# Kernel tuning notes

Hardware: AMD Instinct MI355X
Metric: run time of the kernel (lower is better)

The kernel has to match this reference:

```python
import jax, jax.numpy as jnp
import numpy as np

T, K, D, CIN = 8, 64, 512, 1536  # timesteps, num_centers, redu_dim, input channels


def _conv(x, w, b=None, pad=0):
    y = jax.lax.conv_general_dilated(x, w, (1, 1), [(pad, pad), (pad, pad)],
                                     dimension_numbers=('NCHW', 'OIHW', 'NCHW'))
    return y if b is None else y + b[None, :, None, None]


def setup_inputs() -> dict:
    key = jax.random.key(0)
    ks = jax.random.split(key, 15)
    B, H, W = 32, 8, 8
    s = lambda i, shp: jax.random.normal(ks[i], shp, jnp.float32) * 0.05
    return dict(
        x=jax.random.normal(ks[0], (B * T, CIN, H, W), jnp.float32),
        redu_w=s(1, (D, CIN, 1, 1)), redu_b=s(2, (D,)),
        w_x=s(3, (K, D, 1, 1)),
        att_x=s(4, (K, K, 3, 3)), att_h_w=s(5, (K, K, 3, 3)), att_b=s(6, (K,)),
        share_w=s(7, (K, K, 3, 3)), share_b=s(8, (K,)),
        U_r=s(9, (K, K, 3, 3)), U_z=s(10, (K, K, 3, 3)), U_h=s(11, (K, K, 3, 3)),
        centers=s(12, (K, D)),
        fc1_w=s(13, (T * K // 16, T * K)), fc2_w=s(14, (T * K, T * K // 16)),
    )


def reference(x, redu_w, redu_b, w_x, att_x, att_h_w, att_b, share_w, share_b,
              U_r, U_z, U_h, centers, fc1_w, fc2_w):
    NT, _, H, W = x.shape
    B = NT // T
    xt = _conv(x, redu_w, redu_b)                    # (B*T, D, H, W) 1x1 reduction
    wxpb = _conv(xt, w_x)                            # (B*T, K, H, W)
    att_v = _conv(wxpb, att_x, pad=1).reshape(B, T, K, H, W).transpose(1, 0, 2, 3, 4)  # (T,B,K,H,W)
    wxpb5 = wxpb.reshape(B, T, K, H, W)

    def fc(v):  # ChannelAttention shared MLP (1x1 convs == matmuls)
        return jnp.maximum(v @ fc1_w.T, 0.) @ fc2_w.T

    def step(h, _):
        ah = _conv(h, att_h_w, att_b, pad=1)               # (B,K,H,W)
        e = jax.nn.relu(att_v + ah[None])                  # (T,B,K,H,W)
        e = e.transpose(1, 0, 2, 3, 4).reshape(B, T * K, H * W)
        g = jnp.tanh(fc(e.mean(-1)) + fc(e.max(-1)))       # (B, T*K) channel attention
        ex = jnp.exp(g.reshape(B, T, K))
        den = ex.sum(1, keepdims=True)
        den = den + (den == 0).astype(ex.dtype)
        alphas = ex / den                                  # softmax over timesteps
        wxt = (alphas[:, :, :, None, None] * wxpb5).sum(1) # (B,K,H,W)
        wxt = _conv(wxt, share_w, share_b, pad=1)
        z = jax.nn.sigmoid(wxt + _conv(h, U_z, pad=1))
        r = jax.nn.sigmoid(wxt + _conv(h, U_r, pad=1))
        hh = jnp.tanh(wxt + _conv(r * h, U_h, pad=1))
        h_new = (1. - z) * hh + z * h
        return h_new, h_new

    h0 = jnp.zeros((B, K, H, W), x.dtype)
    _, hs = jax.lax.scan(step, h0, None, length=T)         # (T,B,K,H,W)
    assigns = hs.transpose(1, 0, 2, 3, 4).reshape(B * T, K, H * W)
    a_sum = assigns.sum(-1, keepdims=True)                 # (B*T,K,1)
    a = a_sum * centers[None]                              # (B*T,K,D)
    feats = xt.reshape(B * T, D, H * W).transpose(0, 2, 1) # (B*T,HW,D)
    vlad = jnp.einsum('nks,nsd->nkd', assigns, feats) - a  # (B*T,K,D)
    vlad = vlad.reshape(B, T, K, D).sum(1)                 # (B,K,D)
    vlad = vlad / jnp.maximum(jnp.linalg.norm(vlad, axis=2, keepdims=True), 1e-12)
    vlad = vlad.reshape(B, K * D)
    vlad = vlad / jnp.maximum(jnp.linalg.norm(vlad, axis=1, keepdims=True), 1e-12)
    return vlad
```

## Files before the change

kernel.cpp:

```cpp
#include <hip/hip_runtime.h>
#include <math.h>

#define T_   8
#define K_   64
#define D_   512
#define CIN_ 1536
#define B_   32
#define S_   64
#define NT_  256

#define WLO_BF16  786432u
#define WXT_OFF   786432u
#define XT_OFF    819200u
#define WXPB_OFF  9207808u
#define ATTV_OFF  10256384u
#define HS_OFF    11436032u
#define ASUM_OFF  13041664u
#define WPB       25034752u

typedef __bf16 v8bf __attribute__((ext_vector_type(8)));
typedef __bf16 v4bf __attribute__((ext_vector_type(4)));
typedef float  v4f  __attribute__((ext_vector_type(4)));
typedef _Float16 v4h __attribute__((ext_vector_type(4)));
typedef _Float16 v8h __attribute__((ext_vector_type(8)));

__global__ __launch_bounds__(256) void k_prep(const float* __restrict__ redu_w,
                                              const float* __restrict__ w_x,
                                              float* __restrict__ ws) {
    unsigned idx = blockIdx.x * 256u + threadIdx.x;
    if (idx < 786432u) {
        float f = redu_w[idx];
        __bf16 h = (__bf16)f;
        __bf16 l = (__bf16)(f - (float)h);
        __bf16* wb = (__bf16*)ws;
        wb[idx] = h;
        wb[WLO_BF16 + idx] = l;
    } else if (idx < 819200u) {
        unsigned i = idx - 786432u;
        unsigned dd = i >> 6, k = i & 63u;
        ws[WXT_OFF + i] = w_x[k * 512u + dd];
    }
}

__global__ __launch_bounds__(256) void k_prep_w(const float* __restrict__ w0,
                                                const float* __restrict__ w1,
                                                const float* __restrict__ w2,
                                                const float* __restrict__ w3,
                                                const float* __restrict__ w4,
                                                float* __restrict__ ws) {
    unsigned idx = blockIdx.x * 256u + threadIdx.x;
    if (idx >= 184320u) return;
    unsigned w = idx / 36864u, r = idx % 36864u;
    const float* src = (w == 0) ? w0 : (w == 1) ? w1 : (w == 2) ? w2 : (w == 3) ? w3 : w4;
    float f = src[r];
    __bf16 h = (__bf16)f;
    __bf16 l = (__bf16)(f - (float)h);
    unsigned o = r / 576u, rem = r % 576u, ii = rem / 9u, dydx = rem % 9u;
    __bf16* wb = (__bf16*)ws;
    unsigned dst = WPB + w * 73728u + (dydx * 64u + o) * 64u + ii;
    wb[dst] = h;
    wb[dst + 36864u] = l;
}

__global__ __launch_bounds__(256) void k_gemm_xt_mfma(const float* __restrict__ x,
                                                      const float* __restrict__ redu_b,
                                                      float* __restrict__ ws) {
    __shared__ __bf16 xhi_s[64 * 72];
    __shared__ __bf16 xlo_s[64 * 72];
    const __bf16* __restrict__ Whi = (const __bf16*)ws;
    const __bf16* __restrict__ Wlo = ((const __bf16*)ws) + WLO_BF16;
    float* xt = ws + XT_OFF;
    const int n = blockIdx.y;
    const int d0 = blockIdx.x * 256;
    const int tid = threadIdx.x;
    const int wave = tid >> 6, lane = tid & 63;
    const int lrow = lane & 15, lkg = lane >> 4;
    const int m_base = d0 + wave * 64;
    const float* __restrict__ xn = x + n * 98304;
    const int s4 = tid & 15, cb = tid >> 4;

    v4f acc[4][4];
#pragma unroll
    for (int mt = 0; mt < 4; ++mt)
#pragma unroll
        for (int nt = 0; nt < 4; ++nt) acc[mt][nt] = (v4f){0.f, 0.f, 0.f, 0.f};

    for (int c0 = 0; c0 < 1536; c0 += 64) {
        float4 v[4];
#pragma unroll
        for (int j = 0; j < 4; ++j)
            v[j] = *(const float4*)&xn[(c0 + cb * 4 + j) * 64 + s4 * 4];
        __syncthreads();
#pragma unroll
        for (int i = 0; i < 4; ++i) {
            v4bf hv, lv;
#pragma unroll
            for (int j = 0; j < 4; ++j) {
                float f = ((const float*)&v[j])[i];
                __bf16 h = (__bf16)f;
                hv[j] = h;
                lv[j] = (__bf16)(f - (float)h);
            }
            int row = s4 * 4 + i;
            *(v4bf*)&xhi_s[row * 72 + cb * 4] = hv;
            *(v4bf*)&xlo_s[row * 72 + cb * 4] = lv;
        }
        __syncthreads();
#pragma unroll
        for (int ks = 0; ks < 64; ks += 32) {
            v8bf bh[4], bl[4], ah[4], al[4];
#pragma unroll
            for (int nt = 0; nt < 4; ++nt) {
                int off = (nt * 16 + lrow) * 72 + ks + lkg * 8;
                bh[nt] = *(const v8bf*)&xhi_s[off];
                bl[nt] = *(const v8bf*)&xlo_s[off];
            }
#pragma unroll
            for (int mt = 0; mt < 4; ++mt) {
                int gi = (m_base + mt * 16 + lrow) * 1536 + c0 + ks + lkg * 8;
                ah[mt] = *(const v8bf*)&Whi[gi];
                al[mt] = *(const v8bf*)&Wlo[gi];
            }
#pragma unroll
            for (int mt = 0; mt < 4; ++mt)
#pragma unroll
                for (int nt = 0; nt < 4; ++nt) {
                    acc[mt][nt] = __builtin_amdgcn_mfma_f32_16x16x32_bf16(
                        ah[mt], bh[nt], acc[mt][nt], 0, 0, 0);
                    acc[mt][nt] = __builtin_amdgcn_mfma_f32_16x16x32_bf16(
                        ah[mt], bl[nt], acc[mt][nt], 0, 0, 0);
                    acc[mt][nt] = __builtin_amdgcn_mfma_f32_16x16x32_bf16(
                        al[mt], bh[nt], acc[mt][nt], 0, 0, 0);
                }
        }
    }
#pragma unroll
    for (int mt = 0; mt < 4; ++mt) {
#pragma unroll
        for (int r = 0; r < 4; ++r) {
            int m = m_base + mt * 16 + lkg * 4 + r;
            float bias = redu_b[m];
#pragma unroll
            for (int nt = 0; nt < 4; ++nt) {
                int s = nt * 16 + lrow;
                xt[(n * 512 + m) * 64 + s] = acc[mt][nt][r] + bias;
            }
        }
    }
}

__global__ __launch_bounds__(256) void k_gemm_wxpb(float* __restrict__ ws) {
    __shared__ float Aw[16 * 64];
    __shared__ float Bx[16 * 64];
    const float* wxT = ws + WXT_OFF;
    const float* xt = ws + XT_OFF;
    float* wxpb = ws + WXPB_OFF;
    const int n = blockIdx.x;
    const int tid = threadIdx.x;
    const int sg = tid & 15, kg = tid >> 4;

    float acc[4][4];
#pragma unroll
    for (int i = 0; i < 4; ++i)
#pragma unroll
        for (int j = 0; j < 4; ++j) acc[i][j] = 0.f;

    for (int d0 = 0; d0 < 512; d0 += 16) {
        int cc = tid >> 4, q = tid & 15;
        *(float4*)&Aw[cc * 64 + q * 4] = *(const float4*)&wxT[(d0 + cc) * 64 + q * 4];
        *(float4*)&Bx[cc * 64 + q * 4] = *(const float4*)&xt[n * 32768 + (d0 + cc) * 64 + q * 4];
        __syncthreads();
#pragma unroll
        for (int c2 = 0; c2 < 16; ++c2) {
            float4 a = *(const float4*)&Aw[c2 * 64 + kg * 4];
            float4 b = *(const float4*)&Bx[c2 * 64 + sg * 4];
            float av[4] = {a.x, a.y, a.z, a.w};
            float bv[4] = {b.x, b.y, b.z, b.w};
#pragma unroll
            for (int i = 0; i < 4; ++i)
#pragma unroll
                for (int j = 0; j < 4; ++j)
                    acc[i][j] = fmaf(av[i], bv[j], acc[i][j]);
        }
        __syncthreads();
    }
#pragma unroll
    for (int i = 0; i < 4; ++i) {
        float4 o = {acc[i][0], acc[i][1], acc[i][2], acc[i][3]};
        *(float4*)&wxpb[(n * 64 + kg * 4 + i) * 64 + sg * 4] = o;
    }
}

__global__ __launch_bounds__(128) void k_conv3x3(const float* __restrict__ in,
                                                 const float* __restrict__ wt,
                                                 const float* __restrict__ bias,
                                                 float* __restrict__ out) {
    __shared__ float in_s[4096];
    __shared__ float w_s[16 * 576];
    const int img = blockIdx.y;
    const int k0 = blockIdx.x * 16;
    const int tid = threadIdx.x;
    const int kl = tid >> 3, y = tid & 7;
#pragma unroll
    for (int i = 0; i < 8; ++i) {
        int f = tid + i * 128;
        *(float4*)&in_s[f * 4] = *(const float4*)&in[img * 4096 + f * 4];
    }
#pragma unroll
    for (int i = 0; i < 18; ++i) {
        int f = tid + i * 128;
        *(float4*)&w_s[f * 4] = *(const float4*)&wt[k0 * 576 + f * 4];
    }
    __syncthreads();
    float o[8];
#pragma unroll
    for (int xx = 0; xx < 8; ++xx) o[xx] = 0.f;
    for (int kp = 0; kp < 64; ++kp) {
        const float* wp = &w_s[kl * 576 + kp * 9];
        float wv[9];
#pragma unroll
        for (int q = 0; q < 9; ++q) wv[q] = wp[q];
#pragma unroll
        for (int dy = 0; dy < 3; ++dy) {
            int yy = y + dy - 1;
            if (yy >= 0 && yy < 8) {
                float4 ra = *(const float4*)&in_s[kp * 64 + yy * 8];
                float4 rb = *(const float4*)&in_s[kp * 64 + yy * 8 + 4];
                float r[8] = {ra.x, ra.y, ra.z, ra.w, rb.x, rb.y, rb.z, rb.w};
                float wa = wv[dy * 3 + 0], wb = wv[dy * 3 + 1], wc = wv[dy * 3 + 2];
#pragma unroll
                for (int xx = 0; xx < 8; ++xx) {
                    float t = wb * r[xx];
                    if (xx > 0) t += wa * r[xx - 1];
                    if (xx < 7) t += wc * r[xx + 1];
                    o[xx] += t;
                }
            }
        }
    }
    float bv = bias ? bias[k0 + kl] : 0.f;
    float4 o0 = {o[0] + bv, o[1] + bv, o[2] + bv, o[3] + bv};
    float4 o1 = {o[4] + bv, o[5] + bv, o[6] + bv, o[7] + bv};
    *(float4*)&out[img * 4096 + (k0 + kl) * 64 + y * 8] = o0;
    *(float4*)&out[img * 4096 + (k0 + kl) * 64 + y * 8 + 4] = o1;
}

__device__ __forceinline__ void conv_mfma(const __bf16* __restrict__ Wh,
                                          const __bf16* tS,
                                          int l15, int kg8, int mt, int ntb,
                                          v4f acc[2]) {
    v8bf vz;
#pragma unroll
    for (int q = 0; q < 8; ++q) vz[q] = (__bf16)0.f;
    v4f a0 = (v4f){0.f, 0.f, 0.f, 0.f};
    v4f a1 = (v4f){0.f, 0.f, 0.f, 0.f};
    const int n0 = ntb * 16 + l15;
#pragma unroll
    for (int dy = 0; dy < 3; ++dy) {
        v8bf wh[3][2];
#pragma unroll
        for (int dx = 0; dx < 3; ++dx) {
            const int wrow = ((dy * 3 + dx) * 64 + mt * 16 + l15) * 64 + kg8;
#pragma unroll
            for (int kci = 0; kci < 2; ++kci)
                wh[dx][kci] = *(const v8bf*)&Wh[wrow + kci * 32];
        }
#pragma unroll
        for (int dx = 0; dx < 3; ++dx) {
            const int y0 = (n0 >> 3) + dy - 1, x0 = (n0 & 7) + dx - 1;
            const bool okx = (unsigned)x0 < 8u;
            const bool ok0 = ((unsigned)y0 < 8u) & okx;
            const bool ok1 = ((unsigned)(y0 + 2) < 8u) & okx;
            const int s0 = ((y0 * 8 + x0) & 63) * 72 + kg8;
            const int s1 = (((y0 + 2) * 8 + x0) & 63) * 72 + kg8;
#pragma unroll
            for (int kci = 0; kci < 2; ++kci) {
                v8bf b0 = ok0 ? *(const v8bf*)&tS[s0 + kci * 32] : vz;
                v8bf b1 = ok1 ? *(const v8bf*)&tS[s1 + kci * 32] : vz;
                a0 = __builtin_amdgcn_mfma_f32_16x16x32_bf16(wh[dx][kci], b0, a0, 0, 0, 0);
                a1 = __builtin_amdgcn_mfma_f32_16x16x32_bf16(wh[dx][kci], b1, a1, 0, 0, 0);
            }
        }
    }
    acc[0] = a0;
    acc[1] = a1;
}

__device__ __forceinline__ void conv_mfma3(const __bf16* __restrict__ W0,
                                           const __bf16* __restrict__ W1,
                                           const __bf16* __restrict__ W2,
                                           const __bf16* tS,
                                           int l15, int kg8, int mt, int ntb,
                                           v4f a0[2], v4f a1[2], v4f a2[2]) {
    v8bf vz;
#pragma unroll
    for (int q = 0; q < 8; ++q) vz[q] = (__bf16)0.f;
#pragma unroll
    for (int i = 0; i < 2; ++i) {
        a0[i] = (v4f){0.f, 0.f, 0.f, 0.f};
        a1[i] = (v4f){0.f, 0.f, 0.f, 0.f};
        a2[i] = (v4f){0.f, 0.f, 0.f, 0.f};
    }
    const int n0 = ntb * 16 + l15;
#pragma unroll
    for (int dy = 0; dy < 3; ++dy) {
#pragma unroll
        for (int dx = 0; dx < 3; ++dx) {
            const int wrow = ((dy * 3 + dx) * 64 + mt * 16 + l15) * 64 + kg8;
            v8bf w0[2], w1[2], w2[2];
#pragma unroll
            for (int kci = 0; kci < 2; ++kci) {
                w0[kci] = *(const v8bf*)&W0[wrow + kci * 32];
                w1[kci] = *(const v8bf*)&W1[wrow + kci * 32];
                w2[kci] = *(const v8bf*)&W2[wrow + kci * 32];
            }
            const int y0 = (n0 >> 3) + dy - 1, x0 = (n0 & 7) + dx - 1;
            const bool okx = (unsigned)x0 < 8u;
            const bool ok0 = ((unsigned)y0 < 8u) & okx;
            const bool ok1 = ((unsigned)(y0 + 2) < 8u) & okx;
            const int s0 = ((y0 * 8 + x0) & 63) * 72 + kg8;
            const int s1 = (((y0 + 2) * 8 + x0) & 63) * 72 + kg8;
#pragma unroll
            for (int kci = 0; kci < 2; ++kci) {
                v8bf b0 = ok0 ? *(const v8bf*)&tS[s0 + kci * 32] : vz;
                v8bf b1 = ok1 ? *(const v8bf*)&tS[s1 + kci * 32] : vz;
                a0[0] = __builtin_amdgcn_mfma_f32_16x16x32_bf16(w0[kci], b0, a0[0], 0, 0, 0);
                a0[1] = __builtin_amdgcn_mfma_f32_16x16x32_bf16(w0[kci], b1, a0[1], 0, 0, 0);
                a1[0] = __builtin_amdgcn_mfma_f32_16x16x32_bf16(w1[kci], b0, a1[0], 0, 0, 0);
                a1[1] = __builtin_amdgcn_mfma_f32_16x16x32_bf16(w1[kci], b1, a1[1], 0, 0, 0);
                a2[0] = __builtin_amdgcn_mfma_f32_16x16x32_bf16(w2[kci], b0, a2[0], 0, 0, 0);
                a2[1] = __builtin_amdgcn_mfma_f32_16x16x32_bf16(w2[kci], b1, a2[1], 0, 0, 0);
            }
        }
    }
}

__device__ __forceinline__ void write_c(float* c, const v4f acc[2],
                                        int l15, int kg, int mt, int ntb) {
#pragma unroll
    for (int i = 0; i < 2; ++i)
#pragma unroll
        for (int r = 0; r < 4; ++r)
            c[(mt * 16 + kg * 4 + r) * 65 + (ntb + i) * 16 + l15] = acc[i][r];
}

__global__ __launch_bounds__(512) void k_recur(const float* __restrict__ att_b,
                                               const float* __restrict__ share_b,
                                               const float* __restrict__ fc1_w,
                                               const float* __restrict__ fc2_w,
                                               float* __restrict__ ws) {
    __shared__ float h_s[4096];
    __shared__ __attribute__((aligned(16))) __bf16 tA[64 * 72];
    __shared__ float cA[64 * 65];
    __shared__ float cB[64 * 65];
    __shared__ float misc[1088];
    __shared__ __attribute__((aligned(16))) _Float16 attv_s[32768];
    const int b = blockIdx.x, tid = threadIdx.x;
    const int lane = tid & 63;
    const int wave = tid >> 6, mt = wave >> 1, ntb = (wave & 1) * 2;
    const int l15 = lane & 15, kg = lane >> 4, kg8 = kg * 8;
    const int kk = tid >> 3, yy = tid & 7;
    const __bf16* Wp = (const __bf16*)ws + WPB;
    const float* attv = ws + ATTV_OFF;
    const float* wxpb = ws + WXPB_OFF;
    float* hsg = ws + HS_OFF;
    float* asg = ws + ASUM_OFF;

    {
        const float* src = attv + b * 32768;
        for (int i = tid; i < 8192; i += 512) {
            float4 v = *(const float4*)&src[i * 4];
            v4h h4 = {(_Float16)v.x, (_Float16)v.y, (_Float16)v.z, (_Float16)v.w};
            *(v4h*)&attv_s[i * 4] = h4;
        }
    }

    for (int i = tid; i < 4096; i += 512) h_s[i] = 0.f;
    const float abv = att_b[kk];
    float sb4[4];
#pragma unroll
    for (int r = 0; r < 4; ++r) sb4[r] = share_b[mt * 16 + kg * 4 + r];
    __syncthreads();

    for (int t = 0; t < 8; ++t) {
        {
            int s = tid & 63, g = tid >> 6;
#pragma unroll
            for (int q4 = 0; q4 < 2; ++q4) {
                v4bf hv;
#pragma unroll
                for (int q = 0; q < 4; ++q) hv[q] = (__bf16)h_s[(g * 8 + q4 * 4 + q) * 64 + s];
                *(v4bf*)&tA[s * 72 + g * 8 + q4 * 4] = hv;
            }
        }
        __syncthreads();
        v4f az[2], ar[2];
        {
            v4f a[2];
            conv_mfma3(Wp, Wp + 2u * 73728u, Wp + 3u * 73728u, tA,
                       l15, kg8, mt, ntb, a, az, ar);
            write_c(cA, a, l15, kg, mt, ntb);
        }
        __syncthreads();
        {
            float ah8[8];
            const float* cr = &cA[kk * 65 + yy * 8];
#pragma unroll
            for (int xx = 0; xx < 8; ++xx) ah8[xx] = cr[xx] + abv;
            for (int tp = 0; tp < 8; ++tp) {
                v8h va = *(const v8h*)&attv_s[tp * 4096 + kk * 64 + yy * 8];
                float s_ = 0.f, m_ = 0.f;
#pragma unroll
                for (int xx = 0; xx < 8; ++xx) {
                    float v = fmaxf((float)va[xx] + ah8[xx], 0.f);
                    s_ += v;
                    m_ = fmaxf(m_, v);
                }
                s_ += __shfl_down(s_, 4, 8);
                s_ += __shfl_down(s_, 2, 8);
                s_ += __shfl_down(s_, 1, 8);
                m_ = fmaxf(m_, __shfl_down(m_, 4, 8));
                m_ = fmaxf(m_, __shfl_down(m_, 2, 8));
                m_ = fmaxf(m_, __shfl_down(m_, 1, 8));
                if (yy == 0) {
                    misc[tp * 64 + kk] = s_ * (1.f / 64.f);
                    misc[512 + tp * 64 + kk] = m_;
                }
            }
        }
        __syncthreads();
        {
            int i2 = tid >> 3, part = tid & 7;
            int i = i2 & 31;
            const float* src = misc + ((i2 < 32) ? 0 : 512);
            const float* wrow = fc1_w + i * 512 + part * 64;
            const float* s2 = src + part * 64;
            float p = 0.f;
#pragma unroll
            for (int c4 = 0; c4 < 16; ++c4) {
                float4 wv = *(const float4*)&wrow[c4 * 4];
                float4 sv = *(const float4*)&s2[c4 * 4];
                p = fmaf(wv.x, sv.x, p);
                p = fmaf(wv.y, sv.y, p);
                p = fmaf(wv.z, sv.z, p);
                p = fmaf(wv.w, sv.w, p);
            }
            p += __shfl_down(p, 4, 8);
            p += __shfl_down(p, 2, 8);
            p += __shfl_down(p, 1, 8);
            if (part == 0) misc[1024 + i2] = fmaxf(p, 0.f);
        }
        __syncthreads();
        {
            const float* w2 = fc2_w + tid * 32;
            float gm = 0.f, gx = 0.f;
#pragma unroll
            for (int i4 = 0; i4 < 8; ++i4) {
                float4 wv = *(const float4*)&w2[i4 * 4];
                gm = fmaf(wv.x, misc[1024 + i4 * 4 + 0], gm);
                gm = fmaf(wv.y, misc[1024 + i4 * 4 + 1], gm);
                gm = fmaf(wv.z, misc[1024 + i4 * 4 + 2], gm);
                gm = fmaf(wv.w, misc[1024 + i4 * 4 + 3], gm);
                gx = fmaf(wv.x, misc[1056 + i4 * 4 + 0], gx);
                gx = fmaf(wv.y, misc[1056 + i4 * 4 + 1], gx);
                gx = fmaf(wv.z, misc[1056 + i4 * 4 + 2], gx);
                gx = fmaf(wv.w, misc[1056 + i4 * 4 + 3], gx);
            }
            misc[tid] = expf(tanhf(gm + gx));
        }
        __syncthreads();
        {
            int k6 = tid & 63;
            float den = 0.f;
#pragma unroll
            for (int tp = 0; tp < 8; ++tp) den += misc[tp * 64 + k6];
            den += (den == 0.f) ? 1.f : 0.f;
            misc[512 + tid] = misc[tid] / den;
        }
        __syncthreads();
        {
            float wx8[8];
#pragma unroll
            for (int xx = 0; xx < 8; ++xx) wx8[xx] = 0.f;
            const float* src0 = wxpb + b * 32768 + kk * 64 + yy * 8;
#pragma unroll
            for (int tp = 0; tp < 8; ++tp) {
                float al = misc[512 + tp * 64 + kk];
                float4 v0 = *(const float4*)&src0[tp * 4096];
                float4 v1 = *(const float4*)&src0[tp * 4096 + 4];
                float v[8] = {v0.x, v0.y, v0.z, v0.w, v1.x, v1.y, v1.z, v1.w};
#pragma unroll
                for (int xx = 0; xx < 8; ++xx) wx8[xx] = fmaf(al, v[xx], wx8[xx]);
            }
#pragma unroll
            for (int xx = 0; xx < 8; ++xx) tA[(yy * 8 + xx) * 72 + kk] = (__bf16)wx8[xx];
        }
        __syncthreads();
        v4f ash[2];
        conv_mfma(Wp + 1u * 73728u, tA, l15, kg8, mt, ntb, ash);
        float zf[2][4], wof[2][4];
#pragma unroll
        for (int i = 0; i < 2; ++i)
#pragma unroll
            for (int r = 0; r < 4; ++r) {
                int ko = mt * 16 + kg * 4 + r;
                int s = (ntb + i) * 16 + l15;
                float wo = ash[i][r] + sb4[r];
                float z = 1.f / (1.f + expf(-(wo + az[i][r])));
                float rr = 1.f / (1.f + expf(-(wo + ar[i][r])));
                cB[ko * 65 + s] = rr * h_s[ko * 64 + s];
                zf[i][r] = z;
                wof[i][r] = wo;
            }
        __syncthreads();
        {
            int s = tid & 63, g = tid >> 6;
#pragma unroll
            for (int q4 = 0; q4 < 2; ++q4) {
                v4bf hv;
#pragma unroll
                for (int q = 0; q < 4; ++q) hv[q] = (__bf16)cB[(g * 8 + q4 * 4 + q) * 65 + s];
                *(v4bf*)&tA[s * 72 + g * 8 + q4 * 4] = hv;
            }
        }
        if (tid < 64) misc[1024 + tid] = 0.f;
        __syncthreads();
        v4f ach[2];
        conv_mfma(Wp + 4u * 73728u, tA, l15, kg8, mt, ntb, ach);
#pragma unroll
        for (int r = 0; r < 4; ++r) {
            int ko = mt * 16 + kg * 4 + r;
            float rsum = 0.f;
#pragma unroll
            for (int i = 0; i < 2; ++i) {
                int s = (ntb + i) * 16 + l15;
                float hh = tanhf(wof[i][r] + ach[i][r]);
                float hold = h_s[ko * 64 + s];
                float hn = (1.f - zf[i][r]) * hh + zf[i][r] * hold;
                h_s[ko * 64 + s] = hn;
                hsg[((t * 32 + b) * 64 + ko) * 64 + s] = hn;
                rsum += hn;
            }
            rsum += __shfl_xor(rsum, 8, 16);
            rsum += __shfl_xor(rsum, 4, 16);
            rsum += __shfl_xor(rsum, 2, 16);
            rsum += __shfl_xor(rsum, 1, 16);
            if (l15 == 0) atomicAdd(&misc[1024 + ko], rsum);
        }
        __syncthreads();
        if (tid < 64) asg[b * 512 + t * 64 + tid] = misc[1024 + tid];
        __syncthreads();
    }
}

__global__ __launch_bounds__(256) void k_vlad(const float* __restrict__ centers,
                                              const float* __restrict__ ws,
                                              float* __restrict__ out) {
    __shared__ float As[16 * 68];
    __shared__ float Bs[16 * 68];
    const int b = blockIdx.y;
    const int d0 = blockIdx.x * 64;
    const int tid = threadIdx.x;
    const int kq = tid & 15, dq = tid >> 4;
    const int lk = tid >> 2, q = tid & 3;
    const float* hs = ws + HS_OFF;
    const float* xt = ws + XT_OFF;
    float acc[4][4];
#pragma unroll
    for (int i = 0; i < 4; ++i)
#pragma unroll
        for (int j = 0; j < 4; ++j) acc[i][j] = 0.f;

    for (int rc = 0; rc < 512; rc += 16) {
        int t = rc >> 6, hw0 = rc & 63;
        float4 va = *(const float4*)&hs[((t * 32 + b) * 64 + lk) * 64 + hw0 + q * 4];
        float4 vb = *(const float4*)&xt[(b * 8 + t) * 32768 + (d0 + lk) * 64 + hw0 + q * 4];
        __syncthreads();
        As[(q * 4 + 0) * 68 + lk] = va.x;
        As[(q * 4 + 1) * 68 + lk] = va.y;
        As[(q * 4 + 2) * 68 + lk] = va.z;
        As[(q * 4 + 3) * 68 + lk] = va.w;
        Bs[(q * 4 + 0) * 68 + lk] = vb.x;
        Bs[(q * 4 + 1) * 68 + lk] = vb.y;
        Bs[(q * 4 + 2) * 68 + lk] = vb.z;
        Bs[(q * 4 + 3) * 68 + lk] = vb.w;
        __syncthreads();
#pragma unroll
        for (int cc = 0; cc < 16; ++cc) {
            float4 a = *(const float4*)&As[cc * 68 + kq * 4];
            float4 bb = *(const float4*)&Bs[cc * 68 + dq * 4];
            float av[4] = {a.x, a.y, a.z, a.w};
            float bv[4] = {bb.x, bb.y, bb.z, bb.w};
#pragma unroll
            for (int i = 0; i < 4; ++i)
#pragma unroll
                for (int j = 0; j < 4; ++j)
                    acc[i][j] = fmaf(av[i], bv[j], acc[i][j]);
        }
    }
    const float* asum = ws + ASUM_OFF;
#pragma unroll
    for (int i = 0; i < 4; ++i) {
        int k = kq * 4 + i;
        float at = 0.f;
#pragma unroll
        for (int tp = 0; tp < 8; ++tp) at += asum[b * 512 + tp * 64 + k];
        float4 cen = *(const float4*)&centers[k * 512 + d0 + dq * 4];
        float4 o = {acc[i][0] - at * cen.x, acc[i][1] - at * cen.y,
                    acc[i][2] - at * cen.z, acc[i][3] - at * cen.w};
        *(float4*)&out[b * 32768 + k * 512 + d0 + dq * 4] = o;
    }
}

__global__ __launch_bounds__(64) void k_norm1(float* __restrict__ out) {
    const int b = blockIdx.x >> 6, k = blockIdx.x & 63;
    float* p = out + b * 32768 + k * 512;
    const int tid = threadIdx.x;
    float v[8];
    float ss = 0.f;
#pragma unroll
    for (int i = 0; i < 8; ++i) {
        v[i] = p[tid + i * 64];
        ss = fmaf(v[i], v[i], ss);
    }
#pragma unroll
    for (int off = 32; off > 0; off >>= 1) ss += __shfl_down(ss, off, 64);
    ss = __shfl(ss, 0, 64);
    float sc = 1.f / fmaxf(sqrtf(ss), 1e-12f);
#pragma unroll
    for (int i = 0; i < 8; ++i) p[tid + i * 64] = v[i] * sc;
}

__global__ __launch_bounds__(256) void k_norm2(float* __restrict__ out) {
    __shared__ float red[4];
    __shared__ float stot;
    const int b = blockIdx.x;
    const int tid = threadIdx.x;
    float* p = out + b * 32768;
    float ss = 0.f;
    for (int i = 0; i < 32; ++i) {
        float4 v = *(const float4*)&p[tid * 4 + i * 1024];
        ss += v.x * v.x + v.y * v.y + v.z * v.z + v.w * v.w;
    }
#pragma unroll
    for (int off = 32; off > 0; off >>= 1) ss += __shfl_down(ss, off, 64);
    if ((tid & 63) == 0) red[tid >> 6] = ss;
    __syncthreads();
    if (tid == 0) stot = 1.f / fmaxf(sqrtf(red[0] + red[1] + red[2] + red[3]), 1e-12f);
    __syncthreads();
    float sc = stot;
    for (int i = 0; i < 32; ++i) {
        float4 v = *(const float4*)&p[tid * 4 + i * 1024];
        v.x *= sc; v.y *= sc; v.z *= sc; v.w *= sc;
        *(float4*)&p[tid * 4 + i * 1024] = v;
    }
}

extern "C" void kernel_launch(void* const* d_in, const int* in_sizes, int n_in,
                              void* d_out, int out_size, void* d_ws, size_t ws_size,
                              hipStream_t stream) {
    const float* x       = (const float*)d_in[0];
    const float* redu_w  = (const float*)d_in[1];
    const float* redu_b  = (const float*)d_in[2];
    const float* w_x     = (const float*)d_in[3];
    const float* att_x   = (const float*)d_in[4];
    const float* att_h_w = (const float*)d_in[5];
    const float* att_b   = (const float*)d_in[6];
    const float* share_w = (const float*)d_in[7];
    const float* share_b = (const float*)d_in[8];
    const float* U_r     = (const float*)d_in[9];
    const float* U_z     = (const float*)d_in[10];
    const float* U_h     = (const float*)d_in[11];
    const float* centers = (const float*)d_in[12];
    const float* fc1_w   = (const float*)d_in[13];
    const float* fc2_w   = (const float*)d_in[14];
    float* ws = (float*)d_ws;
    float* out = (float*)d_out;

    k_prep<<<dim3(3200), dim3(256), 0, stream>>>(redu_w, w_x, ws);
    k_prep_w<<<dim3(720), dim3(256), 0, stream>>>(att_h_w, share_w, U_z, U_r, U_h, ws);
    k_gemm_xt_mfma<<<dim3(2, 256), dim3(256), 0, stream>>>(x, redu_b, ws);
    k_gemm_wxpb<<<dim3(256), dim3(256), 0, stream>>>(ws);
    k_conv3x3<<<dim3(4, 256), dim3(128), 0, stream>>>(ws + WXPB_OFF, att_x,
                                                      (const float*)nullptr, ws + ATTV_OFF);
    k_recur<<<dim3(32), dim3(512), 0, stream>>>(att_b, share_b, fc1_w, fc2_w, ws);
    k_vlad<<<dim3(8, 32), dim3(256), 0, stream>>>(centers, ws, out);
    k_norm1<<<dim3(2048), dim3(64), 0, stream>>>(out);
    k_norm2<<<dim3(32), dim3(256), 0, stream>>>(out);
}
```

Measured before the change: 752.0 us.

## Halve recurrence block to 4 waves, each covering all 64 spatial columns

```diff
diff --git a/kernel.cpp b/kernel.cpp
--- a/kernel.cpp
+++ b/kernel.cpp
@@ -247,104 +247,93 @@
 
 __device__ __forceinline__ void conv_mfma(const __bf16* __restrict__ Wh,
                                           const __bf16* tS,
-                                          int l15, int kg8, int mt, int ntb,
-                                          v4f acc[2]) {
+                                          int l15, int kg8, int mt, v4f acc[4]) {
     v8bf vz;
 #pragma unroll
     for (int q = 0; q < 8; ++q) vz[q] = (__bf16)0.f;
-    v4f a0 = (v4f){0.f, 0.f, 0.f, 0.f};
-    v4f a1 = (v4f){0.f, 0.f, 0.f, 0.f};
-    const int n0 = ntb * 16 + l15;
-#pragma unroll
-    for (int dy = 0; dy < 3; ++dy) {
-        v8bf wh[3][2];
+#pragma unroll
+    for (int i = 0; i < 4; ++i) acc[i] = (v4f){0.f, 0.f, 0.f, 0.f};
+    const int yb = l15 >> 3, xb = l15 & 7;
+    v8bf wh[9][2];
+#pragma unroll
+    for (int p = 0; p < 9; ++p) {
+        const int wrow = (p * 64 + mt * 16 + l15) * 64 + kg8;
+#pragma unroll
+        for (int kci = 0; kci < 2; ++kci)
+            wh[p][kci] = *(const v8bf*)&Wh[wrow + kci * 32];
+    }
+#pragma unroll
+    for (int dy = 0; dy < 3; ++dy)
 #pragma unroll
         for (int dx = 0; dx < 3; ++dx) {
-            const int wrow = ((dy * 3 + dx) * 64 + mt * 16 + l15) * 64 + kg8;
-#pragma unroll
-            for (int kci = 0; kci < 2; ++kci)
-                wh[dx][kci] = *(const v8bf*)&Wh[wrow + kci * 32];
-        }
-#pragma unroll
-        for (int dx = 0; dx < 3; ++dx) {
-            const int y0 = (n0 >> 3) + dy - 1, x0 = (n0 & 7) + dx - 1;
+            const int x0 = xb + dx - 1;
             const bool okx = (unsigned)x0 < 8u;
-            const bool ok0 = ((unsigned)y0 < 8u) & okx;
-            const bool ok1 = ((unsigned)(y0 + 2) < 8u) & okx;
-            const int s0 = ((y0 * 8 + x0) & 63) * 72 + kg8;
-            const int s1 = (((y0 + 2) * 8 + x0) & 63) * 72 + kg8;
-#pragma unroll
-            for (int kci = 0; kci < 2; ++kci) {
-                v8bf b0 = ok0 ? *(const v8bf*)&tS[s0 + kci * 32] : vz;
-                v8bf b1 = ok1 ? *(const v8bf*)&tS[s1 + kci * 32] : vz;
-                a0 = __builtin_amdgcn_mfma_f32_16x16x32_bf16(wh[dx][kci], b0, a0, 0, 0, 0);
-                a1 = __builtin_amdgcn_mfma_f32_16x16x32_bf16(wh[dx][kci], b1, a1, 0, 0, 0);
-            }
-        }
-    }
-    acc[0] = a0;
-    acc[1] = a1;
+#pragma unroll
+            for (int i = 0; i < 4; ++i) {
+                const int y0 = yb + dy - 1 + 2 * i;
+                const bool ok = ((unsigned)y0 < 8u) & okx;
+                const int s0 = ((y0 * 8 + x0) & 63) * 72 + kg8;
+#pragma unroll
+                for (int kci = 0; kci < 2; ++kci) {
+                    v8bf b = ok ? *(const v8bf*)&tS[s0 + kci * 32] : vz;
+                    acc[i] = __builtin_amdgcn_mfma_f32_16x16x32_bf16(
+                        wh[dy * 3 + dx][kci], b, acc[i], 0, 0, 0);
+                }
+            }
+        }
 }
 
 __device__ __forceinline__ void conv_mfma3(const __bf16* __restrict__ W0,
                                            const __bf16* __restrict__ W1,
                                            const __bf16* __restrict__ W2,
                                            const __bf16* tS,
-                                           int l15, int kg8, int mt, int ntb,
-                                           v4f a0[2], v4f a1[2], v4f a2[2]) {
+                                           int l15, int kg8, int mt,
+                                           v4f a0[4], v4f a1[4], v4f a2[4]) {
     v8bf vz;
 #pragma unroll
     for (int q = 0; q < 8; ++q) vz[q] = (__bf16)0.f;
 #pragma unroll
-    for (int i = 0; i < 2; ++i) {
+    for (int i = 0; i < 4; ++i) {
         a0[i] = (v4f){0.f, 0.f, 0.f, 0.f};
         a1[i] = (v4f){0.f, 0.f, 0.f, 0.f};
         a2[i] = (v4f){0.f, 0.f, 0.f, 0.f};
     }
-    const int n0 = ntb * 16 + l15;
+    const int yb = l15 >> 3, xb = l15 & 7;
 #pragma unroll
     for (int dy = 0; dy < 3; ++dy) {
+        v8bf w0[3][2], w1[3][2], w2[3][2];
 #pragma unroll
         for (int dx = 0; dx < 3; ++dx) {
             const int wrow = ((dy * 3 + dx) * 64 + mt * 16 + l15) * 64 + kg8;
-            v8bf w0[2], w1[2], w2[2];
 #pragma unroll
             for (int kci = 0; kci < 2; ++kci) {
-                w0[kci] = *(const v8bf*)&W0[wrow + kci * 32];
-                w1[kci] = *(const v8bf*)&W1[wrow + kci * 32];
-                w2[kci] = *(const v8bf*)&W2[wrow + kci * 32];
-            }
-            const int y0 = (n0 >> 3) + dy - 1, x0 = (n0 & 7) + dx - 1;
+                w0[dx][kci] = *(const v8bf*)&W0[wrow + kci * 32];
+                w1[dx][kci] = *(const v8bf*)&W1[wrow + kci * 32];
+                w2[dx][kci] = *(const v8bf*)&W2[wrow + kci * 32];
+            }
+        }
+#pragma unroll
+        for (int dx = 0; dx < 3; ++dx) {
+            const int x0 = xb + dx - 1;
             const bool okx = (unsigned)x0 < 8u;
-            const bool ok0 = ((unsigned)y0 < 8u) & okx;
-            const bool ok1 = ((unsigned)(y0 + 2) < 8u) & okx;
-            const int s0 = ((y0 * 8 + x0) & 63) * 72 + kg8;
-            const int s1 = (((y0 + 2) * 8 + x0) & 63) * 72 + kg8;
-#pragma unroll
-            for (int kci = 0; kci < 2; ++kci) {
-                v8bf b0 = ok0 ? *(const v8bf*)&tS[s0 + kci * 32] : vz;
-                v8bf b1 = ok1 ? *(const v8bf*)&tS[s1 + kci * 32] : vz;
-                a0[0] = __builtin_amdgcn_mfma_f32_16x16x32_bf16(w0[kci], b0, a0[0], 0, 0, 0);
-                a0[1] = __builtin_amdgcn_mfma_f32_16x16x32_bf16(w0[kci], b1, a0[1], 0, 0, 0);
-                a1[0] = __builtin_amdgcn_mfma_f32_16x16x32_bf16(w1[kci], b0, a1[0], 0, 0, 0);
-                a1[1] = __builtin_amdgcn_mfma_f32_16x16x32_bf16(w1[kci], b1, a1[1], 0, 0, 0);
-                a2[0] = __builtin_amdgcn_mfma_f32_16x16x32_bf16(w2[kci], b0, a2[0], 0, 0, 0);
-                a2[1] = __builtin_amdgcn_mfma_f32_16x16x32_bf16(w2[kci], b1, a2[1], 0, 0, 0);
-            }
-        }
-    }
-}
-
-__device__ __forceinline__ void write_c(float* c, const v4f acc[2],
-                                        int l15, int kg, int mt, int ntb) {
-#pragma unroll
-    for (int i = 0; i < 2; ++i)
-#pragma unroll
-        for (int r = 0; r < 4; ++r)
-            c[(mt * 16 + kg * 4 + r) * 65 + (ntb + i) * 16 + l15] = acc[i][r];
-}
-
-__global__ __launch_bounds__(512) void k_recur(const float* __restrict__ att_b,
+#pragma unroll
+            for (int i = 0; i < 4; ++i) {
+                const int y0 = yb + dy - 1 + 2 * i;
+                const bool ok = ((unsigned)y0 < 8u) & okx;
+                const int s0 = ((y0 * 8 + x0) & 63) * 72 + kg8;
+#pragma unroll
+                for (int kci = 0; kci < 2; ++kci) {
+                    v8bf b = ok ? *(const v8bf*)&tS[s0 + kci * 32] : vz;
+                    a0[i] = __builtin_amdgcn_mfma_f32_16x16x32_bf16(w0[dx][kci], b, a0[i], 0, 0, 0);
+                    a1[i] = __builtin_amdgcn_mfma_f32_16x16x32_bf16(w1[dx][kci], b, a1[i], 0, 0, 0);
+                    a2[i] = __builtin_amdgcn_mfma_f32_16x16x32_bf16(w2[dx][kci], b, a2[i], 0, 0, 0);
+                }
+            }
+        }
+    }
+}
+
+__global__ __launch_bounds__(256) void k_recur(const float* __restrict__ att_b,
                                                const float* __restrict__ share_b,
                                                const float* __restrict__ fc1_w,
                                                const float* __restrict__ fc2_w,
@@ -357,9 +346,9 @@
     __shared__ __attribute__((aligned(16))) _Float16 attv_s[32768];
     const int b = blockIdx.x, tid = threadIdx.x;
     const int lane = tid & 63;
-    const int wave = tid >> 6, mt = wave >> 1, ntb = (wave & 1) * 2;
+    const int wave = tid >> 6;
+    const int mt = wave;
     const int l15 = lane & 15, kg = lane >> 4, kg8 = kg * 8;
-    const int kk = tid >> 3, yy = tid & 7;
     const __bf16* Wp = (const __bf16*)ws + WPB;
     const float* attv = ws + ATTV_OFF;
     const float* wxpb = ws + WXPB_OFF;
@@ -368,23 +357,26 @@
 
     {
         const float* src = attv + b * 32768;
-        for (int i = tid; i < 8192; i += 512) {
+        for (int i = tid; i < 8192; i += 256) {
             float4 v = *(const float4*)&src[i * 4];
             v4h h4 = {(_Float16)v.x, (_Float16)v.y, (_Float16)v.z, (_Float16)v.w};
             *(v4h*)&attv_s[i * 4] = h4;
         }
     }
 
-    for (int i = tid; i < 4096; i += 512) h_s[i] = 0.f;
-    const float abv = att_b[kk];
+    for (int i = tid; i < 4096; i += 256) h_s[i] = 0.f;
+    float abvr[2];
+#pragma unroll
+    for (int rep = 0; rep < 2; ++rep) abvr[rep] = att_b[(tid + rep * 256) >> 3];
     float sb4[4];
 #pragma unroll
     for (int r = 0; r < 4; ++r) sb4[r] = share_b[mt * 16 + kg * 4 + r];
     __syncthreads();
 
     for (int t = 0; t < 8; ++t) {
-        {
-            int s = tid & 63, g = tid >> 6;
+#pragma unroll
+        for (int rep = 0; rep < 2; ++rep) {
+            int s = tid & 63, g = (tid >> 6) + rep * 4;
 #pragma unroll
             for (int q4 = 0; q4 < 2; ++q4) {
                 v4bf hv;
@@ -394,19 +386,26 @@
             }
         }
         __syncthreads();
-        v4f az[2], ar[2];
+        v4f az[4], ar[4];
         {
-            v4f a[2];
+            v4f a[4];
             conv_mfma3(Wp, Wp + 2u * 73728u, Wp + 3u * 73728u, tA,
-                       l15, kg8, mt, ntb, a, az, ar);
-            write_c(cA, a, l15, kg, mt, ntb);
-        }
-        __syncthreads();
-        {
+                       l15, kg8, mt, a, az, ar);
+#pragma unroll
+            for (int i = 0; i < 4; ++i)
+#pragma unroll
+                for (int r = 0; r < 4; ++r)
+                    cA[(mt * 16 + kg * 4 + r) * 65 + i * 16 + l15] = a[i][r];
+        }
+        __syncthreads();
+#pragma unroll
+        for (int rep = 0; rep < 2; ++rep) {
+            int vt = tid + rep * 256;
+            int kk = vt >> 3, yy = vt & 7;
             float ah8[8];
             const float* cr = &cA[kk * 65 + yy * 8];
 #pragma unroll
-            for (int xx = 0; xx < 8; ++xx) ah8[xx] = cr[xx] + abv;
+            for (int xx = 0; xx < 8; ++xx) ah8[xx] = cr[xx] + abvr[rep];
             for (int tp = 0; tp < 8; ++tp) {
                 v8h va = *(const v8h*)&attv_s[tp * 4096 + kk * 64 + yy * 8];
                 float s_ = 0.f, m_ = 0.f;
@@ -430,14 +429,14 @@
         }
         __syncthreads();
         {
-            int i2 = tid >> 3, part = tid & 7;
+            int i2 = tid >> 2, part = tid & 3;
             int i = i2 & 31;
             const float* src = misc + ((i2 < 32) ? 0 : 512);
-            const float* wrow = fc1_w + i * 512 + part * 64;
-            const float* s2 = src + part * 64;
+            const float* wrow = fc1_w + i * 512 + part * 128;
+            const float* s2 = src + part * 128;
             float p = 0.f;
 #pragma unroll
-            for (int c4 = 0; c4 < 16; ++c4) {
+            for (int c4 = 0; c4 < 32; ++c4) {
                 float4 wv = *(const float4*)&wrow[c4 * 4];
                 float4 sv = *(const float4*)&s2[c4 * 4];
                 p = fmaf(wv.x, sv.x, p);
@@ -445,14 +444,15 @@
                 p = fmaf(wv.z, sv.z, p);
                 p = fmaf(wv.w, sv.w, p);
             }
-            p += __shfl_down(p, 4, 8);
-            p += __shfl_down(p, 2, 8);
-            p += __shfl_down(p, 1, 8);
+            p += __shfl_down(p, 2, 4);
+            p += __shfl_down(p, 1, 4);
             if (part == 0) misc[1024 + i2] = fmaxf(p, 0.f);
         }
         __syncthreads();
-        {
-            const float* w2 = fc2_w + tid * 32;
+#pragma unroll
+        for (int rep = 0; rep < 2; ++rep) {
+            int vt = tid + rep * 256;
+            const float* w2 = fc2_w + vt * 32;
             float gm = 0.f, gx = 0.f;
 #pragma unroll
             for (int i4 = 0; i4 < 8; ++i4) {
@@ -466,19 +466,24 @@
                 gx = fmaf(wv.z, misc[1056 + i4 * 4 + 2], gx);
                 gx = fmaf(wv.w, misc[1056 + i4 * 4 + 3], gx);
             }
-            misc[tid] = expf(tanhf(gm + gx));
-        }
-        __syncthreads();
-        {
-            int k6 = tid & 63;
+            misc[vt] = expf(tanhf(gm + gx));
+        }
+        __syncthreads();
+#pragma unroll
+        for (int rep = 0; rep < 2; ++rep) {
+            int vt = tid + rep * 256;
+            int k6 = vt & 63;
             float den = 0.f;
 #pragma unroll
             for (int tp = 0; tp < 8; ++tp) den += misc[tp * 64 + k6];
             den += (den == 0.f) ? 1.f : 0.f;
-            misc[512 + tid] = misc[tid] / den;
-        }
-        __syncthreads();
-        {
+            misc[512 + vt] = misc[vt] / den;
+        }
+        __syncthreads();
+#pragma unroll
+        for (int rep = 0; rep < 2; ++rep) {
+            int vt = tid + rep * 256;
+            int kk = vt >> 3, yy = vt & 7;
             float wx8[8];
 #pragma unroll
             for (int xx = 0; xx < 8; ++xx) wx8[xx] = 0.f;
@@ -496,15 +501,15 @@
             for (int xx = 0; xx < 8; ++xx) tA[(yy * 8 + xx) * 72 + kk] = (__bf16)wx8[xx];
         }
         __syncthreads();
-        v4f ash[2];
-        conv_mfma(Wp + 1u * 73728u, tA, l15, kg8, mt, ntb, ash);
-        float zf[2][4], wof[2][4];
-#pragma unroll
-        for (int i = 0; i < 2; ++i)
+        v4f ash[4];
+        conv_mfma(Wp + 1u * 73728u, tA, l15, kg8, mt, ash);
+        float zf[4][4], wof[4][4];
+#pragma unroll
+        for (int i = 0; i < 4; ++i)
 #pragma unroll
             for (int r = 0; r < 4; ++r) {
                 int ko = mt * 16 + kg * 4 + r;
-                int s = (ntb + i) * 16 + l15;
+                int s = i * 16 + l15;
                 float wo = ash[i][r] + sb4[r];
                 float z = 1.f / (1.f + expf(-(wo + az[i][r])));
                 float rr = 1.f / (1.f + expf(-(wo + ar[i][r])));
@@ -513,8 +518,9 @@
                 wof[i][r] = wo;
             }
         __syncthreads();
-        {
-            int s = tid & 63, g = tid >> 6;
+#pragma unroll
+        for (int rep = 0; rep < 2; ++rep) {
+            int s = tid & 63, g = (tid >> 6) + rep * 4;
 #pragma unroll
             for (int q4 = 0; q4 < 2; ++q4) {
                 v4bf hv;
@@ -523,29 +529,30 @@
                 *(v4bf*)&tA[s * 72 + g * 8 + q4 * 4] = hv;
             }
         }
-        if (tid < 64) misc[1024 + tid] = 0.f;
-        __syncthreads();
-        v4f ach[2];
-        conv_mfma(Wp + 4u * 73728u, tA, l15, kg8, mt, ntb, ach);
-#pragma unroll
-        for (int r = 0; r < 4; ++r) {
-            int ko = mt * 16 + kg * 4 + r;
-            float rsum = 0.f;
-#pragma unroll
-            for (int i = 0; i < 2; ++i) {
-                int s = (ntb + i) * 16 + l15;
-                float hh = tanhf(wof[i][r] + ach[i][r]);
-                float hold = h_s[ko * 64 + s];
-                float hn = (1.f - zf[i][r]) * hh + zf[i][r] * hold;
-                h_s[ko * 64 + s] = hn;
-                hsg[((t * 32 + b) * 64 + ko) * 64 + s] = hn;
-                rsum += hn;
-            }
-            rsum += __shfl_xor(rsum, 8, 16);
-            rsum += __shfl_xor(rsum, 4, 16);
-            rsum += __shfl_xor(rsum, 2, 16);
-            rsum += __shfl_xor(rsum, 1, 16);
-            if (l15 == 0) atomicAdd(&misc[1024 + ko], rsum);
+        __syncthreads();
+        {
+            v4f ach[4];
+            conv_mfma(Wp + 4u * 73728u, tA, l15, kg8, mt, ach);
+#pragma unroll
+            for (int r = 0; r < 4; ++r) {
+                int ko = mt * 16 + kg * 4 + r;
+                float rsum = 0.f;
+#pragma unroll
+                for (int i = 0; i < 4; ++i) {
+                    int s = i * 16 + l15;
+                    float hh = tanhf(wof[i][r] + ach[i][r]);
+                    float hold = h_s[ko * 64 + s];
+                    float hn = (1.f - zf[i][r]) * hh + zf[i][r] * hold;
+                    h_s[ko * 64 + s] = hn;
+                    hsg[((t * 32 + b) * 64 + ko) * 64 + s] = hn;
+                    rsum += hn;
+                }
+                rsum += __shfl_xor(rsum, 8, 16);
+                rsum += __shfl_xor(rsum, 4, 16);
+                rsum += __shfl_xor(rsum, 2, 16);
+                rsum += __shfl_xor(rsum, 1, 16);
+                if (l15 == 0) misc[1024 + ko] = rsum;
+            }
         }
         __syncthreads();
         if (tid < 64) asg[b * 512 + t * 64 + tid] = misc[1024 + tid];
@@ -683,7 +690,7 @@
     k_gemm_wxpb<<<dim3(256), dim3(256), 0, stream>>>(ws);
     k_conv3x3<<<dim3(4, 256), dim3(128), 0, stream>>>(ws + WXPB_OFF, att_x,
                                                       (const float*)nullptr, ws + ATTV_OFF);
-    k_recur<<<dim3(32), dim3(512), 0, stream>>>(att_b, share_b, fc1_w, fc2_w, ws);
+    k_recur<<<dim3(32), dim3(256), 0, stream>>>(att_b, share_b, fc1_w, fc2_w, ws);
     k_vlad<<<dim3(8, 32), dim3(256), 0, stream>>>(centers, ws, out);
     k_norm1<<<dim3(2048), dim3(64), 0, stream>>>(out);
     k_norm2<<<dim3(32), dim3(256), 0, stream>>>(out);
```

Result: no change. 737.7 us (-1.9%).
